# Performance work log

Hardware: AMD Instinct MI355X
Metric: run time of the kernel (lower is better)

Reference implementation:

```python
import jax, jax.numpy as jnp
import numpy as np

DIM = 256
HID = DIM * 16

def setup_inputs() -> dict:
    key = jax.random.key(0)
    ks = jax.random.split(key, 6)
    B, L = 4, 2048
    x = jax.random.normal(ks[0], (B, L, DIM), dtype=jnp.float32)
    # nn.Linear(dim, hidden): weight [H, D], bias [H]
    WB = jax.random.normal(ks[1], (HID, DIM), dtype=jnp.float32) / np.sqrt(DIM)
    bB = jax.random.normal(ks[2], (HID,), dtype=jnp.float32) * 0.01
    # nn.Linear(hidden, dim): weight [D, H], bias [D]
    WC = jax.random.normal(ks[3], (DIM, HID), dtype=jnp.float32) / np.sqrt(HID)
    bC = jax.random.normal(ks[4], (DIM,), dtype=jnp.float32) * 0.01
    A = jax.random.normal(ks[5], (HID,), dtype=jnp.float32)
    return {"x": x, "WB": WB, "bB": bB, "WC": WC, "bC": bC, "A": A}

def reference(x, WB, bB, WC, bC, A):
    # b = B(x): [B, L, H]
    b = jnp.einsum('bld,hd->blh', x, WB) + bB
    a = jax.nn.sigmoid(A)  # [H], time-invariant decay
    # h_t = a * h_{t-1} + b_t  (h_0 from zero state) -> associative scan over L
    a_seq = jnp.broadcast_to(a, b.shape)
    def comb(c1, c2):
        a1, u1 = c1
        a2, u2 = c2
        return (a1 * a2, a2 * u1 + u2)
    _, h = jax.lax.associative_scan(comb, (a_seq, b), axis=1)  # [B, L, H]
    # C(h): [B, L, D]
    return jnp.einsum('blh,dh->bld', h, WC) + bC
```

## Files before the change

### kernel.cpp

```cpp
#include <hip/hip_runtime.h>
#include <hip/hip_bf16.h>

#define DIMSZ 256
#define HID 4096
#define BATCH 4
#define SEQ 2048
#define NCH 64
#define CLEN 32
#define SPLITK2 4
#define KCHUNK (HID / SPLITK2)
#define BM2 64

typedef __bf16 bf16_t;
typedef __bf16 bf16x4 __attribute__((ext_vector_type(4)));
typedef __bf16 bf16x8 __attribute__((ext_vector_type(8)));
typedef float  f32x4  __attribute__((ext_vector_type(4)));

__device__ __forceinline__ float sigmoidf_dev(float x) {
    return 1.0f / (1.0f + __expf(-x));
}

__device__ __forceinline__ void load_lds16(const bf16_t* g, bf16_t* l) {
    __builtin_amdgcn_global_load_lds(
        (const __attribute__((address_space(1))) void*)g,
        (__attribute__((address_space(3))) void*)l,
        16, 0, 0);
}

__device__ __forceinline__ bf16x8 cvt8(const float* p) {
    bf16x8 o;
    #pragma unroll
    for (int j = 0; j < 8; j++) o[j] = (bf16_t)p[j];
    return o;
}

__global__ void prep_kernel(const float* __restrict__ x,
                            const float* __restrict__ WB,
                            const float* __restrict__ WC,
                            bf16_t* __restrict__ xt,
                            bf16_t* __restrict__ WBt,
                            bf16_t* __restrict__ Wt) {
    int i = blockIdx.x * blockDim.x + threadIdx.x;
    if (i < 262144) {
        int lane = i & 63, m16 = (i >> 6) & 511, ks = i >> 15;
        int row = m16 * 16 + (lane & 15);
        int k   = ks * 32 + (lane >> 4) * 8;
        *(bf16x8*)&xt[(size_t)i * 8] = cvt8(&x[(size_t)row * DIMSZ + k]);
    } else if (i < 393216) {
        int j = i - 262144;
        int lane = j & 63, n16 = (j >> 6) & 255, ks = j >> 14;
        int row = n16 * 16 + (lane & 15);
        int k   = ks * 32 + (lane >> 4) * 8;
        *(bf16x8*)&WBt[(size_t)j * 8] = cvt8(&WB[(size_t)row * DIMSZ + k]);
    } else {
        int j = i - 393216;
        int lane = j & 63, g = (j >> 6) & 15, ks = j >> 10;
        int row = g * 16 + (lane & 15);
        int k   = ks * 32 + (lane >> 4) * 8;
        *(bf16x8*)&Wt[(size_t)j * 8] = cvt8(&WC[(size_t)row * HID + k]);
    }
}

__global__ __launch_bounds__(256)
void gemm1_fused(const bf16_t* __restrict__ xt, const bf16_t* __restrict__ WBt,
                 const float* __restrict__ bias, const float* __restrict__ Adecay,
                 bf16_t* __restrict__ Cg, float* __restrict__ totals)
{
    constexpr int LDT = 136;
    __shared__ bf16_t tile[128 * LDT];

    const int tid = threadIdx.x, wave = tid >> 6, lane = tid & 63;
    const int wm = wave >> 1, wn = wave & 1, q = lane >> 4, r16 = lane & 15;
    const int mBase = blockIdx.x * 128, nBase = blockIdx.y * 128;
    const int m16Base = blockIdx.x * 8 + wm * 4;
    const int n16Base = blockIdx.y * 8 + wn * 4;
    const int batch = mBase >> 11, tIn = mBase & 2047;

    f32x4 acc[4][4] = {};

    #pragma unroll 2
    for (int ks = 0; ks < 8; ks++) {
        bf16x8 af[4], bfr[4];
        #pragma unroll
        for (int mt = 0; mt < 4; mt++)
            af[mt] = *(const bf16x8*)&xt[(((size_t)ks * 512 + m16Base + mt) * 64 + lane) * 8];
        #pragma unroll
        for (int nt = 0; nt < 4; nt++)
            bfr[nt] = *(const bf16x8*)&WBt[(((size_t)ks * 256 + n16Base + nt) * 64 + lane) * 8];
        #pragma unroll
        for (int mt = 0; mt < 4; mt++)
            #pragma unroll
            for (int nt = 0; nt < 4; nt++)
                acc[mt][nt] = __builtin_amdgcn_mfma_f32_16x16x32_bf16(
                    af[mt], bfr[nt], acc[mt][nt], 0, 0, 0);
    }

    #pragma unroll
    for (int nt = 0; nt < 4; nt++) {
        const int chl = wn * 64 + nt * 16 + r16;
        const float bv = bias[nBase + chl];
        #pragma unroll
        for (int mt = 0; mt < 4; mt++) {
            const int t0 = wm * 64 + mt * 16 + q * 4;
            bf16x4 pk;
            #pragma unroll
            for (int rg = 0; rg < 4; rg++)
                pk[rg] = (bf16_t)(acc[mt][nt][rg] + bv);
            *(bf16x4*)&tile[chl * LDT + t0] = pk;
        }
    }
    __syncthreads();

    #pragma unroll
    for (int p = 0; p < 8; p++) {
        const int task = p * 256 + tid;
        const int ch = task >> 4, o = task & 15;
        *(bf16x8*)&Cg[((size_t)batch * HID + nBase + ch) * SEQ + tIn + o * 8] =
            *(const bf16x8*)&tile[ch * LDT + o * 8];
    }

    #pragma unroll
    for (int t = 0; t < 2; t++) {
        const int task = tid + t * 256;
        const int ch = task & 127, ck = task >> 7;
        const float a = sigmoidf_dev(Adecay[nBase + ch]);
        float tot = 0.f;
        #pragma unroll
        for (int o = 0; o < 4; o++) {
            bf16x8 v8 = *(const bf16x8*)&tile[ch * LDT + ck * CLEN + o * 8];
            #pragma unroll
            for (int j = 0; j < 8; j++)
                tot = a * tot + (float)v8[j];
        }
        const int cg = (tIn >> 5) + ck;
        totals[(size_t)(batch * NCH + cg) * HID + nBase + ch] = tot;
    }
}

__global__ void scan_carries_kernel(const float* __restrict__ totals,
                                    const float* __restrict__ Adecay,
                                    float* __restrict__ carries)
{
    int gid = blockIdx.x * 64 + threadIdx.x;
    int ch    = gid & (HID - 1);
    int batch = gid >> 12;
    float a = sigmoidf_dev(Adecay[ch]);
    float aC = a;
    #pragma unroll
    for (int i = 0; i < 5; i++) aC *= aC;

    float v[NCH];
    #pragma unroll
    for (int c = 0; c < NCH; c++)
        v[c] = totals[(size_t)(batch * NCH + c) * HID + ch];

    float carry = 0.f;
    #pragma unroll
    for (int c = 0; c < NCH; c++) {
        carries[(size_t)(batch * NCH + c) * HID + ch] = carry;
        carry = aC * carry + v[c];
    }
}

__global__ __launch_bounds__(256, 2)
void gemm2_fused(const bf16_t* __restrict__ bv, const bf16_t* __restrict__ Wt,
                 const float* __restrict__ Adecay, const float* __restrict__ carries,
                 bf16_t* __restrict__ P)
{
    constexpr int CKSTRIDE = BM2 * 32 + 32;
    __shared__ bf16_t hs[16896];
    __shared__ bf16_t hs2[16384];

    const int tid = threadIdx.x, wave = tid >> 6, lane = tid & 63;
    const int q = lane >> 4, r16 = lane & 15;
    const int mBase = blockIdx.x * BM2;
    const int kBase = blockIdx.y * KCHUNK;
    const int batch = mBase >> 11, tIn = mBase & 2047;
    const int chunk0 = tIn >> 5;

    const int srcOct = ((lane & 7) - (lane >> 3)) & 7;

    float aD[4], sd0[4], sd1[4];
    #pragma unroll
    for (int s = 0; s < 4; s++) {
        const int c = kBase + s * 256 + tid;
        aD[s]  = Adecay[c];
        sd0[s] = carries[(size_t)(batch * NCH + chunk0) * HID + c];
        sd1[s] = carries[(size_t)(batch * NCH + chunk0 + 1) * HID + c];
    }

    f32x4 acc[4][4] = {};

    {
        const size_t rowBase = (size_t)batch * HID + kBase;
        #pragma unroll
        for (int i = 0; i < 8; i++) {
            const int g = wave * 8 + i;
            load_lds16(&bv[(rowBase + g * 8 + (lane >> 3)) * SEQ + tIn + srcOct * 8],
                       &hs2[g * 512]);
        }
    }

    #pragma unroll
    for (int s = 0; s < 4; s++) {
        __syncthreads();

        {
            const float a = sigmoidf_dev(aD[s]);
            float st0 = sd0[s], st1 = sd1[s];
            const int rot = tid & 7;
            bf16_t* hw = &hs[(tid >> 5) * CKSTRIDE + (tid & 31)];
            const bf16_t* hr = &hs2[tid * 64];
            #pragma unroll
            for (int k = 0; k < 4; k++) {
                bf16x8 va = *(const bf16x8*)&hr[(((k + rot) & 7)) << 3];
                bf16x8 vb = *(const bf16x8*)&hr[(((k + 4 + rot) & 7)) << 3];
                #pragma unroll
                for (int j = 0; j < 8; j++) {
                    st0 = a * st0 + (float)va[j];
                    st1 = a * st1 + (float)vb[j];
                    hw[(k * 8 + j) * 32]        = (bf16_t)st0;
                    hw[((k + 4) * 8 + j) * 32]  = (bf16_t)st1;
                }
            }
        }
        __syncthreads();

        if (s < 3) {
            const size_t rowBase = (size_t)batch * HID + kBase + (s + 1) * 256;
            #pragma unroll
            for (int i = 0; i < 8; i++) {
                const int g = wave * 8 + i;
                load_lds16(&bv[(rowBase + g * 8 + (lane >> 3)) * SEQ + tIn + srcOct * 8],
                           &hs2[g * 512]);
            }
        }

        const int ksBase = (kBase >> 5) + s * 8;
        #pragma unroll 2
        for (int cki = 0; cki < 8; cki++) {
            bf16x8 af[4], bfr[4];
            #pragma unroll
            for (int nt = 0; nt < 4; nt++)
                bfr[nt] = *(const bf16x8*)&Wt[
                    (((size_t)(ksBase + cki) * 16 + wave * 4 + nt) * 64 + lane) * 8];
            #pragma unroll
            for (int mt = 0; mt < 4; mt++)
                af[mt] = *(const bf16x8*)&hs[cki * CKSTRIDE + (mt * 16 + r16) * 32 + q * 8];
            #pragma unroll
            for (int mt = 0; mt < 4; mt++)
                #pragma unroll
                for (int nt = 0; nt < 4; nt++)
                    acc[mt][nt] = __builtin_amdgcn_mfma_f32_16x16x32_bf16(
                        af[mt], bfr[nt], acc[mt][nt], 0, 0, 0);
        }
    }

    __syncthreads();
    #pragma unroll
    for (int nt = 0; nt < 4; nt++) {
        const int col = wave * 64 + nt * 16 + r16;
        #pragma unroll
        for (int mt = 0; mt < 4; mt++)
            #pragma unroll
            for (int rg = 0; rg < 4; rg++)
                hs[(mt * 16 + q * 4 + rg) * 264 + col] = (bf16_t)acc[mt][nt][rg];
    }
    __syncthreads();

    bf16_t* Pb = P + (size_t)blockIdx.y * (BATCH * SEQ) * DIMSZ;
    #pragma unroll
    for (int p = 0; p < 8; p++) {
        int task = p * 256 + tid;
        int r = task >> 5, g8 = (task & 31) << 3;
        *(bf16x8*)&Pb[(size_t)(mBase + r) * DIMSZ + g8] =
            *(const bf16x8*)&hs[r * 264 + g8];
    }
}

__global__ void reduce_out_kernel(const bf16_t* __restrict__ P,
                                  const float* __restrict__ bias,
                                  float* __restrict__ out, int nTask) {
    int i = blockIdx.x * blockDim.x + threadIdx.x;
    if (i >= nTask) return;
    int n8 = (i & 31) << 3;
    size_t off = (size_t)i * 8;
    float v[8];
    #pragma unroll
    for (int j = 0; j < 8; j++) v[j] = bias[n8 + j];
    #pragma unroll
    for (int sp = 0; sp < SPLITK2; sp++) {
        bf16x8 p = *(const bf16x8*)&P[(size_t)sp * (BATCH * SEQ) * DIMSZ + off];
        #pragma unroll
        for (int j = 0; j < 8; j++) v[j] += (float)p[j];
    }
    float4* o4 = (float4*)&out[off];
    o4[0] = make_float4(v[0], v[1], v[2], v[3]);
    o4[1] = make_float4(v[4], v[5], v[6], v[7]);
}

extern "C" void kernel_launch(void* const* d_in, const int* in_sizes, int n_in,
                              void* d_out, int out_size, void* d_ws, size_t ws_size,
                              hipStream_t stream)
{
    const float* x  = (const float*)d_in[0];
    const float* WB = (const float*)d_in[1];
    const float* bB = (const float*)d_in[2];
    const float* WC = (const float*)d_in[3];
    const float* bC = (const float*)d_in[4];
    const float* A  = (const float*)d_in[5];

    char* ws = (char*)d_ws;
    size_t off = 0;
    bf16_t* xt   = (bf16_t*)(ws + off); off += (size_t)BATCH * SEQ * DIMSZ * 2;
    bf16_t* WBt  = (bf16_t*)(ws + off); off += (size_t)HID * DIMSZ * 2;
    bf16_t* Wt   = (bf16_t*)(ws + off); off += (size_t)DIMSZ * HID * 2;
    bf16_t* bbuf = (bf16_t*)(ws + off); off += (size_t)BATCH * SEQ * HID * 2;
    bf16_t* partials = (bf16_t*)(ws + off); off += (size_t)SPLITK2 * BATCH * SEQ * DIMSZ * 2;
    float* totals   = (float*)(ws + off); off += (size_t)BATCH * NCH * HID * 4;
    float* carries  = (float*)(ws + off); off += (size_t)BATCH * NCH * HID * 4;

    const int M = BATCH * SEQ;

    prep_kernel<<<2048, 256, 0, stream>>>(x, WB, WC, xt, WBt, Wt);

    dim3 g1(M / 128, HID / 128);
    gemm1_fused<<<g1, 256, 0, stream>>>(xt, WBt, bB, A, bbuf, totals);

    scan_carries_kernel<<<256, 64, 0, stream>>>(totals, A, carries);

    dim3 g2(M / BM2, SPLITK2);
    gemm2_fused<<<g2, 256, 0, stream>>>(bbuf, Wt, A, carries, partials);

    int nTask = M * DIMSZ / 8;
    reduce_out_kernel<<<(nTask + 255) / 256, 256, 0, stream>>>(
        partials, bC, (float*)d_out, nTask);
}
```

Measured before the change: 141.4 us.

## Store gemm1 output chunk-major and pipeline gemm2 scan with register double buffering

gemm1 now writes the B projection in a chunk-major layout ([batch][chunk][HID][32]), so each gemm2 thread reads its 32-step slice as contiguous 16-byte vectors. gemm2 drops to 32-row tiles (one scan chunk) and replaces global_load_lds staging with register prefetch of the next slab. The scanned slabs are double-buffered in LDS, which removes one barrier per slab and shrinks shared memory enough to raise the occupancy target to 4 blocks. The trade-off is that each WC tile is re-read by twice as many blocks, and each block has fewer MFMAs to hide latency behind.

```diff
diff --git a/kernel.cpp b/kernel.cpp
--- a/kernel.cpp
+++ b/kernel.cpp
@@ -9,7 +9,7 @@
 #define CLEN 32
 #define SPLITK2 4
 #define KCHUNK (HID / SPLITK2)
-#define BM2 64
+#define BM2 32
 
 typedef __bf16 bf16_t;
 typedef __bf16 bf16x4 __attribute__((ext_vector_type(4)));
@@ -18,13 +18,6 @@
 
 __device__ __forceinline__ float sigmoidf_dev(float x) {
     return 1.0f / (1.0f + __expf(-x));
-}
-
-__device__ __forceinline__ void load_lds16(const bf16_t* g, bf16_t* l) {
-    __builtin_amdgcn_global_load_lds(
-        (const __attribute__((address_space(1))) void*)g,
-        (__attribute__((address_space(3))) void*)l,
-        16, 0, 0);
 }
 
 __device__ __forceinline__ bf16x8 cvt8(const float* p) {
@@ -75,6 +68,7 @@
     const int m16Base = blockIdx.x * 8 + wm * 4;
     const int n16Base = blockIdx.y * 8 + wn * 4;
     const int batch = mBase >> 11, tIn = mBase & 2047;
+    const int cg0 = tIn >> 5;
 
     f32x4 acc[4][4] = {};
 
@@ -115,7 +109,8 @@
     for (int p = 0; p < 8; p++) {
         const int task = p * 256 + tid;
         const int ch = task >> 4, o = task & 15;
-        *(bf16x8*)&Cg[((size_t)batch * HID + nBase + ch) * SEQ + tIn + o * 8] =
+        const int cc = o >> 2, oo = o & 3;
+        *(bf16x8*)&Cg[((size_t)(batch * NCH + cg0 + cc) * HID + nBase + ch) * 32 + oo * 8] =
             *(const bf16x8*)&tile[ch * LDT + o * 8];
     }
 
@@ -132,8 +127,7 @@
             for (int j = 0; j < 8; j++)
                 tot = a * tot + (float)v8[j];
         }
-        const int cg = (tIn >> 5) + ck;
-        totals[(size_t)(batch * NCH + cg) * HID + nBase + ch] = tot;
+        totals[(size_t)(batch * NCH + cg0 + ck) * HID + nBase + ch] = tot;
     }
 }
 
@@ -162,119 +156,117 @@
     }
 }
 
-__global__ __launch_bounds__(256, 2)
+#define SCAN_SLAB(REG, S)                                                   \
+    do {                                                                    \
+        const float a = sigmoidf_dev(aD[S]);                                \
+        float st = sd[S];                                                   \
+        bf16_t* hw = &hs[(S) & 1][(tid >> 5) * CKSTRIDE + (tid & 31)];      \
+        _Pragma("unroll")                                                   \
+        for (int o = 0; o < 4; o++) {                                       \
+            _Pragma("unroll")                                               \
+            for (int j = 0; j < 8; j++) {                                   \
+                st = a * st + (float)REG[o][j];                             \
+                hw[(o * 8 + j) * 32] = (bf16_t)st;                          \
+            }                                                               \
+        }                                                                   \
+    } while (0)
+
+__global__ __launch_bounds__(256, 4)
 void gemm2_fused(const bf16_t* __restrict__ bv, const bf16_t* __restrict__ Wt,
                  const float* __restrict__ Adecay, const float* __restrict__ carries,
                  bf16_t* __restrict__ P)
 {
-    constexpr int CKSTRIDE = BM2 * 32 + 32;
-    __shared__ bf16_t hs[16896];
-    __shared__ bf16_t hs2[16384];
+    constexpr int CKSTRIDE = CLEN * 32 + 32;
+    __shared__ bf16_t hs[2][8 * CKSTRIDE];
 
     const int tid = threadIdx.x, wave = tid >> 6, lane = tid & 63;
     const int q = lane >> 4, r16 = lane & 15;
     const int mBase = blockIdx.x * BM2;
     const int kBase = blockIdx.y * KCHUNK;
     const int batch = mBase >> 11, tIn = mBase & 2047;
-    const int chunk0 = tIn >> 5;
-
-    const int srcOct = ((lane & 7) - (lane >> 3)) & 7;
-
-    float aD[4], sd0[4], sd1[4];
+    const int chunk = tIn >> 5;
+
+    const size_t rowBase = ((size_t)(batch * NCH + chunk) * HID + kBase + tid) * 32;
+
+    bf16x8 rA[4], rB[4];
+    #pragma unroll
+    for (int o = 0; o < 4; o++)
+        rA[o] = *(const bf16x8*)&bv[rowBase + o * 8];
+
+    float aD[4], sd[4];
     #pragma unroll
     for (int s = 0; s < 4; s++) {
         const int c = kBase + s * 256 + tid;
-        aD[s]  = Adecay[c];
-        sd0[s] = carries[(size_t)(batch * NCH + chunk0) * HID + c];
-        sd1[s] = carries[(size_t)(batch * NCH + chunk0 + 1) * HID + c];
-    }
-
-    f32x4 acc[4][4] = {};
-
-    {
-        const size_t rowBase = (size_t)batch * HID + kBase;
-        #pragma unroll
-        for (int i = 0; i < 8; i++) {
-            const int g = wave * 8 + i;
-            load_lds16(&bv[(rowBase + g * 8 + (lane >> 3)) * SEQ + tIn + srcOct * 8],
-                       &hs2[g * 512]);
-        }
-    }
-
-    #pragma unroll
-    for (int s = 0; s < 4; s++) {
-        __syncthreads();
-
-        {
-            const float a = sigmoidf_dev(aD[s]);
-            float st0 = sd0[s], st1 = sd1[s];
-            const int rot = tid & 7;
-            bf16_t* hw = &hs[(tid >> 5) * CKSTRIDE + (tid & 31)];
-            const bf16_t* hr = &hs2[tid * 64];
-            #pragma unroll
-            for (int k = 0; k < 4; k++) {
-                bf16x8 va = *(const bf16x8*)&hr[(((k + rot) & 7)) << 3];
-                bf16x8 vb = *(const bf16x8*)&hr[(((k + 4 + rot) & 7)) << 3];
-                #pragma unroll
-                for (int j = 0; j < 8; j++) {
-                    st0 = a * st0 + (float)va[j];
-                    st1 = a * st1 + (float)vb[j];
-                    hw[(k * 8 + j) * 32]        = (bf16_t)st0;
-                    hw[((k + 4) * 8 + j) * 32]  = (bf16_t)st1;
-                }
-            }
-        }
-        __syncthreads();
-
-        if (s < 3) {
-            const size_t rowBase = (size_t)batch * HID + kBase + (s + 1) * 256;
-            #pragma unroll
-            for (int i = 0; i < 8; i++) {
-                const int g = wave * 8 + i;
-                load_lds16(&bv[(rowBase + g * 8 + (lane >> 3)) * SEQ + tIn + srcOct * 8],
-                           &hs2[g * 512]);
-            }
-        }
-
+        aD[s] = Adecay[c];
+        sd[s] = carries[(size_t)(batch * NCH + chunk) * HID + c];
+    }
+
+    f32x4 acc[2][4] = {};
+
+    auto mfma_phase = [&](const bf16_t* hb, int s) {
         const int ksBase = (kBase >> 5) + s * 8;
         #pragma unroll 2
         for (int cki = 0; cki < 8; cki++) {
-            bf16x8 af[4], bfr[4];
+            bf16x8 af[2], bfr[4];
             #pragma unroll
             for (int nt = 0; nt < 4; nt++)
                 bfr[nt] = *(const bf16x8*)&Wt[
                     (((size_t)(ksBase + cki) * 16 + wave * 4 + nt) * 64 + lane) * 8];
             #pragma unroll
-            for (int mt = 0; mt < 4; mt++)
-                af[mt] = *(const bf16x8*)&hs[cki * CKSTRIDE + (mt * 16 + r16) * 32 + q * 8];
-            #pragma unroll
-            for (int mt = 0; mt < 4; mt++)
+            for (int mt = 0; mt < 2; mt++)
+                af[mt] = *(const bf16x8*)&hb[cki * CKSTRIDE + (mt * 16 + r16) * 32 + q * 8];
+            #pragma unroll
+            for (int mt = 0; mt < 2; mt++)
                 #pragma unroll
                 for (int nt = 0; nt < 4; nt++)
                     acc[mt][nt] = __builtin_amdgcn_mfma_f32_16x16x32_bf16(
                         af[mt], bfr[nt], acc[mt][nt], 0, 0, 0);
         }
-    }
-
-    __syncthreads();
+    };
+
+    #pragma unroll
+    for (int o = 0; o < 4; o++)
+        rB[o] = *(const bf16x8*)&bv[rowBase + 1 * 8192 + o * 8];
+    SCAN_SLAB(rA, 0);
+    __syncthreads();
+    mfma_phase(&hs[0][0], 0);
+
+    #pragma unroll
+    for (int o = 0; o < 4; o++)
+        rA[o] = *(const bf16x8*)&bv[rowBase + 2 * 8192 + o * 8];
+    SCAN_SLAB(rB, 1);
+    __syncthreads();
+    mfma_phase(&hs[1][0], 1);
+
+    #pragma unroll
+    for (int o = 0; o < 4; o++)
+        rB[o] = *(const bf16x8*)&bv[rowBase + 3 * 8192 + o * 8];
+    SCAN_SLAB(rA, 2);
+    __syncthreads();
+    mfma_phase(&hs[0][0], 2);
+
+    SCAN_SLAB(rB, 3);
+    __syncthreads();
+    mfma_phase(&hs[1][0], 3);
+
     #pragma unroll
     for (int nt = 0; nt < 4; nt++) {
         const int col = wave * 64 + nt * 16 + r16;
         #pragma unroll
-        for (int mt = 0; mt < 4; mt++)
+        for (int mt = 0; mt < 2; mt++)
             #pragma unroll
             for (int rg = 0; rg < 4; rg++)
-                hs[(mt * 16 + q * 4 + rg) * 264 + col] = (bf16_t)acc[mt][nt][rg];
+                hs[0][(mt * 16 + q * 4 + rg) * 264 + col] = (bf16_t)acc[mt][nt][rg];
     }
     __syncthreads();
 
     bf16_t* Pb = P + (size_t)blockIdx.y * (BATCH * SEQ) * DIMSZ;
     #pragma unroll
-    for (int p = 0; p < 8; p++) {
+    for (int p = 0; p < 4; p++) {
         int task = p * 256 + tid;
         int r = task >> 5, g8 = (task & 31) << 3;
         *(bf16x8*)&Pb[(size_t)(mBase + r) * DIMSZ + g8] =
-            *(const bf16x8*)&hs[r * 264 + g8];
+            *(const bf16x8*)&hs[0][r * 264 + g8];
     }
 }
 
```

Measured after the change: 140.0 us. About the same (-1.0%).

## Recompute first GEMM inside second GEMM instead of storing intermediate b

Applied to the files above, without the earlier changes.

The first GEMM now only produces per-chunk totals and no longer writes the full bf16 B(x) intermediate (B*L*H) to global memory. The second GEMM recomputes its B(x) tile with MFMA from xt and WBt for each 256-channel sub-chunk, applies the bias, scans it in LDS and feeds it to the output GEMM. LDS layouts get XOR swizzles to avoid bank conflicts. This removes a 64 MB write and read of the intermediate, at the cost of computing the first GEMM twice.

```diff
diff --git a/kernel.cpp b/kernel.cpp
--- a/kernel.cpp
+++ b/kernel.cpp
@@ -18,13 +18,6 @@
 
 __device__ __forceinline__ float sigmoidf_dev(float x) {
     return 1.0f / (1.0f + __expf(-x));
-}
-
-__device__ __forceinline__ void load_lds16(const bf16_t* g, bf16_t* l) {
-    __builtin_amdgcn_global_load_lds(
-        (const __attribute__((address_space(1))) void*)g,
-        (__attribute__((address_space(3))) void*)l,
-        16, 0, 0);
 }
 
 __device__ __forceinline__ bf16x8 cvt8(const float* p) {
@@ -62,9 +55,9 @@
 }
 
 __global__ __launch_bounds__(256)
-void gemm1_fused(const bf16_t* __restrict__ xt, const bf16_t* __restrict__ WBt,
-                 const float* __restrict__ bias, const float* __restrict__ Adecay,
-                 bf16_t* __restrict__ Cg, float* __restrict__ totals)
+void gemm1_totals(const bf16_t* __restrict__ xt, const bf16_t* __restrict__ WBt,
+                  const float* __restrict__ bias, const float* __restrict__ Adecay,
+                  float* __restrict__ totals)
 {
     constexpr int LDT = 136;
     __shared__ bf16_t tile[128 * LDT];
@@ -75,6 +68,7 @@
     const int m16Base = blockIdx.x * 8 + wm * 4;
     const int n16Base = blockIdx.y * 8 + wn * 4;
     const int batch = mBase >> 11, tIn = mBase & 2047;
+    const int cg0 = tIn >> 5;
 
     f32x4 acc[4][4] = {};
 
@@ -110,14 +104,6 @@
         }
     }
     __syncthreads();
-
-    #pragma unroll
-    for (int p = 0; p < 8; p++) {
-        const int task = p * 256 + tid;
-        const int ch = task >> 4, o = task & 15;
-        *(bf16x8*)&Cg[((size_t)batch * HID + nBase + ch) * SEQ + tIn + o * 8] =
-            *(const bf16x8*)&tile[ch * LDT + o * 8];
-    }
 
     #pragma unroll
     for (int t = 0; t < 2; t++) {
@@ -132,8 +118,7 @@
             for (int j = 0; j < 8; j++)
                 tot = a * tot + (float)v8[j];
         }
-        const int cg = (tIn >> 5) + ck;
-        totals[(size_t)(batch * NCH + cg) * HID + nBase + ch] = tot;
+        totals[(size_t)(batch * NCH + cg0 + ck) * HID + nBase + ch] = tot;
     }
 }
 
@@ -163,13 +148,15 @@
 }
 
 __global__ __launch_bounds__(256, 2)
-void gemm2_fused(const bf16_t* __restrict__ bv, const bf16_t* __restrict__ Wt,
+void gemm2_fused(const bf16_t* __restrict__ xt, const bf16_t* __restrict__ WBt,
+                 const bf16_t* __restrict__ Wt, const float* __restrict__ biasB,
                  const float* __restrict__ Adecay, const float* __restrict__ carries,
                  bf16_t* __restrict__ P)
 {
     constexpr int CKSTRIDE = BM2 * 32 + 32;
-    __shared__ bf16_t hs[16896];
-    __shared__ bf16_t hs2[16384];
+    constexpr int LDB = 72;
+    __shared__ bf16_t bs[256 * LDB];
+    __shared__ bf16_t hs[8 * CKSTRIDE];
 
     const int tid = threadIdx.x, wave = tid >> 6, lane = tid & 63;
     const int q = lane >> 4, r16 = lane & 15;
@@ -177,8 +164,7 @@
     const int kBase = blockIdx.y * KCHUNK;
     const int batch = mBase >> 11, tIn = mBase & 2047;
     const int chunk0 = tIn >> 5;
-
-    const int srcOct = ((lane & 7) - (lane >> 3)) & 7;
+    const int m16B = mBase >> 4;
 
     float aD[4], sd0[4], sd1[4];
     #pragma unroll
@@ -189,52 +175,70 @@
         sd1[s] = carries[(size_t)(batch * NCH + chunk0 + 1) * HID + c];
     }
 
-    f32x4 acc[4][4] = {};
-
-    {
-        const size_t rowBase = (size_t)batch * HID + kBase;
-        #pragma unroll
-        for (int i = 0; i < 8; i++) {
-            const int g = wave * 8 + i;
-            load_lds16(&bv[(rowBase + g * 8 + (lane >> 3)) * SEQ + tIn + srcOct * 8],
-                       &hs2[g * 512]);
-        }
-    }
+    f32x4 accC[4][4] = {};
 
     #pragma unroll
     for (int s = 0; s < 4; s++) {
+        f32x4 accB[4][4] = {};
+        const int n16B = (kBase >> 4) + s * 16 + wave * 4;
+        #pragma unroll 2
+        for (int ks = 0; ks < 8; ks++) {
+            bf16x8 af[4], bfr[4];
+            #pragma unroll
+            for (int mt = 0; mt < 4; mt++)
+                af[mt] = *(const bf16x8*)&xt[(((size_t)ks * 512 + m16B + mt) * 64 + lane) * 8];
+            #pragma unroll
+            for (int nt = 0; nt < 4; nt++)
+                bfr[nt] = *(const bf16x8*)&WBt[(((size_t)ks * 256 + n16B + nt) * 64 + lane) * 8];
+            #pragma unroll
+            for (int mt = 0; mt < 4; mt++)
+                #pragma unroll
+                for (int nt = 0; nt < 4; nt++)
+                    accB[mt][nt] = __builtin_amdgcn_mfma_f32_16x16x32_bf16(
+                        af[mt], bfr[nt], accB[mt][nt], 0, 0, 0);
+        }
+
+        __syncthreads();
+
+        #pragma unroll
+        for (int nt = 0; nt < 4; nt++) {
+            const int chl = wave * 64 + nt * 16 + r16;
+            const float bv = biasB[kBase + s * 256 + chl];
+            const int cx = (chl >> 3) & 7;
+            #pragma unroll
+            for (int mt = 0; mt < 4; mt++) {
+                const int oct = (mt * 2 + (q >> 1)) ^ cx;
+                bf16x4 pk;
+                #pragma unroll
+                for (int rg = 0; rg < 4; rg++)
+                    pk[rg] = (bf16_t)(accB[mt][nt][rg] + bv);
+                *(bf16x4*)&bs[chl * LDB + oct * 8 + (q & 1) * 4] = pk;
+            }
+        }
         __syncthreads();
 
         {
             const float a = sigmoidf_dev(aD[s]);
             float st0 = sd0[s], st1 = sd1[s];
-            const int rot = tid & 7;
-            bf16_t* hw = &hs[(tid >> 5) * CKSTRIDE + (tid & 31)];
-            const bf16_t* hr = &hs2[tid * 64];
-            #pragma unroll
-            for (int k = 0; k < 4; k++) {
-                bf16x8 va = *(const bf16x8*)&hr[(((k + rot) & 7)) << 3];
-                bf16x8 vb = *(const bf16x8*)&hr[(((k + 4 + rot) & 7)) << 3];
+            const int rx = (tid >> 3) & 7;
+            bf16x8 va[8];
+            #pragma unroll
+            for (int o = 0; o < 8; o++)
+                va[o] = *(const bf16x8*)&bs[tid * LDB + ((o ^ rx) << 3)];
+            bf16_t* hw = &hs[(tid >> 5) * CKSTRIDE];
+            const int cho = (tid >> 3) & 3, chi = tid & 7;
+            #pragma unroll
+            for (int o = 0; o < 4; o++)
                 #pragma unroll
                 for (int j = 0; j < 8; j++) {
-                    st0 = a * st0 + (float)va[j];
-                    st1 = a * st1 + (float)vb[j];
-                    hw[(k * 8 + j) * 32]        = (bf16_t)st0;
-                    hw[((k + 4) * 8 + j) * 32]  = (bf16_t)st1;
+                    const int t0 = o * 8 + j, t1 = t0 + 32;
+                    st0 = a * st0 + (float)va[o][j];
+                    hw[t0 * 32 + ((cho ^ ((t0 >> 2) & 3)) << 3) + chi] = (bf16_t)st0;
+                    st1 = a * st1 + (float)va[o + 4][j];
+                    hw[t1 * 32 + ((cho ^ ((t1 >> 2) & 3)) << 3) + chi] = (bf16_t)st1;
                 }
-            }
         }
         __syncthreads();
-
-        if (s < 3) {
-            const size_t rowBase = (size_t)batch * HID + kBase + (s + 1) * 256;
-            #pragma unroll
-            for (int i = 0; i < 8; i++) {
-                const int g = wave * 8 + i;
-                load_lds16(&bv[(rowBase + g * 8 + (lane >> 3)) * SEQ + tIn + srcOct * 8],
-                           &hs2[g * 512]);
-            }
-        }
 
         const int ksBase = (kBase >> 5) + s * 8;
         #pragma unroll 2
@@ -246,17 +250,17 @@
                     (((size_t)(ksBase + cki) * 16 + wave * 4 + nt) * 64 + lane) * 8];
             #pragma unroll
             for (int mt = 0; mt < 4; mt++)
-                af[mt] = *(const bf16x8*)&hs[cki * CKSTRIDE + (mt * 16 + r16) * 32 + q * 8];
+                af[mt] = *(const bf16x8*)&hs[cki * CKSTRIDE + (mt * 16 + r16) * 32
+                                             + ((q ^ (r16 >> 2)) << 3)];
             #pragma unroll
             for (int mt = 0; mt < 4; mt++)
                 #pragma unroll
                 for (int nt = 0; nt < 4; nt++)
-                    acc[mt][nt] = __builtin_amdgcn_mfma_f32_16x16x32_bf16(
-                        af[mt], bfr[nt], acc[mt][nt], 0, 0, 0);
-        }
-    }
-
-    __syncthreads();
+                    accC[mt][nt] = __builtin_amdgcn_mfma_f32_16x16x32_bf16(
+                        af[mt], bfr[nt], accC[mt][nt], 0, 0, 0);
+        }
+    }
+
     #pragma unroll
     for (int nt = 0; nt < 4; nt++) {
         const int col = wave * 64 + nt * 16 + r16;
@@ -264,17 +268,17 @@
         for (int mt = 0; mt < 4; mt++)
             #pragma unroll
             for (int rg = 0; rg < 4; rg++)
-                hs[(mt * 16 + q * 4 + rg) * 264 + col] = (bf16_t)acc[mt][nt][rg];
+                bs[(mt * 16 + q * 4 + rg) * 264 + col] = (bf16_t)accC[mt][nt][rg];
     }
     __syncthreads();
 
     bf16_t* Pb = P + (size_t)blockIdx.y * (BATCH * SEQ) * DIMSZ;
     #pragma unroll
     for (int p = 0; p < 8; p++) {
-        int task = p * 256 + tid;
-        int r = task >> 5, g8 = (task & 31) << 3;
+        const int task = p * 256 + tid;
+        const int r = task >> 5, g8 = (task & 31) << 3;
         *(bf16x8*)&Pb[(size_t)(mBase + r) * DIMSZ + g8] =
-            *(const bf16x8*)&hs[r * 264 + g8];
+            *(const bf16x8*)&bs[r * 264 + g8];
     }
 }
 
@@ -315,7 +319,6 @@
     bf16_t* xt   = (bf16_t*)(ws + off); off += (size_t)BATCH * SEQ * DIMSZ * 2;
     bf16_t* WBt  = (bf16_t*)(ws + off); off += (size_t)HID * DIMSZ * 2;
     bf16_t* Wt   = (bf16_t*)(ws + off); off += (size_t)DIMSZ * HID * 2;
-    bf16_t* bbuf = (bf16_t*)(ws + off); off += (size_t)BATCH * SEQ * HID * 2;
     bf16_t* partials = (bf16_t*)(ws + off); off += (size_t)SPLITK2 * BATCH * SEQ * DIMSZ * 2;
     float* totals   = (float*)(ws + off); off += (size_t)BATCH * NCH * HID * 4;
     float* carries  = (float*)(ws + off); off += (size_t)BATCH * NCH * HID * 4;
@@ -325,12 +328,12 @@
     prep_kernel<<<2048, 256, 0, stream>>>(x, WB, WC, xt, WBt, Wt);
 
     dim3 g1(M / 128, HID / 128);
-    gemm1_fused<<<g1, 256, 0, stream>>>(xt, WBt, bB, A, bbuf, totals);
+    gemm1_totals<<<g1, 256, 0, stream>>>(xt, WBt, bB, A, totals);
 
     scan_carries_kernel<<<256, 64, 0, stream>>>(totals, A, carries);
 
     dim3 g2(M / BM2, SPLITK2);
-    gemm2_fused<<<g2, 256, 0, stream>>>(bbuf, Wt, A, carries, partials);
+    gemm2_fused<<<g2, 256, 0, stream>>>(xt, WBt, Wt, bB, A, carries, partials);
 
     int nTask = M * DIMSZ / 8;
     reduce_out_kernel<<<(nTask + 255) / 256, 256, 0, stream>>>(
```

Measured after the change: 151.7 us. 1.07x slower.
